# Optimization experiments

Measured on AMD Instinct MI355X. Metric: run time of the kernel, lower is better.

The kernel has to match this reference:

```python
import jax, jax.numpy as jnp
import numpy as np

BATCH = 4096
IN_DIM = 512
OUT_DIM = 512
GRID_SIZE = 5
K = 3


def _extended_grid():
    # Original: grid = linspace(-1, 1, grid_size+1), spacing h = 2/grid_size.
    # The de Boor-Cox recursion in the source indexes up to grid[grid_size+2k],
    # so we extend the uniform grid to the right with the same spacing.
    h = 2.0 / GRID_SIZE
    return (-1.0 + h * jnp.arange(GRID_SIZE + 2 * K + 1)).astype(jnp.float32)


def bspline_basis(x, grid, k):
    """Vectorized de Boor-Cox recursion.
    x: [..., ] floats; returns basis [..., grid_size + k].
    Identical math to the recursive b_spline_basis in the source, but computed
    bottom-up over all knot intervals at once (no redundant recomputation).
    """
    xe = x[..., None]  # [..., 1]
    # degree-0: indicator of half-open knot intervals, [..., n_knots-1]
    B = ((grid[:-1] <= xe) & (xe < grid[1:])).astype(x.dtype)
    for d in range(1, k + 1):
        n = grid.shape[0] - d - 1
        gi, gid = grid[:n], grid[d:d + n]          # grid[i], grid[i+d]
        gi1, gid1 = grid[1:n + 1], grid[d + 1:d + n + 1]  # grid[i+1], grid[i+d+1]
        # uniform grid -> denominators are d*h, never zero
        B = (xe - gi) / (gid - gi) * B[..., :n] + (gid1 - xe) / (gid1 - gi1) * B[..., 1:n + 1]
    return B  # [..., grid_size + k]


def setup_inputs() -> dict:
    key = jax.random.key(0)
    k1, k2 = jax.random.split(key)
    x = jax.random.uniform(k1, (BATCH, IN_DIM), jnp.float32) * 2.0 - 1.0  # in [-1, 1)
    spline_coeff = jax.random.normal(k2, (IN_DIM, OUT_DIM, GRID_SIZE + K), jnp.float32)
    spline_scaling = jnp.ones((IN_DIM, OUT_DIM), jnp.float32)
    return {"x": x, "spline_coeff": spline_coeff, "spline_scaling": spline_scaling}


def reference(x, spline_coeff, spline_scaling):
    grid = _extended_grid()
    basis = bspline_basis(x, grid, K)  # [B, in_dim, grid_size+k]
    # out[b, j] = sum_i scaling[i,j] * sum_g basis[b,i,g] * coeff[i,j,g]
    return jnp.einsum('big,ijg,ij->bj', basis, spline_coeff, spline_scaling)
```

## Files before the change

### kernel.cpp

```cpp
#include <hip/hip_runtime.h>
#include <hip/hip_bf16.h>
#include <stdint.h>


#define BATCH   4096
#define IN_DIM  512
#define OUT_DIM 512
#define KDIM    (IN_DIM * 8)
#define SPLITK  4
#define KSPAN   (KDIM / SPLITK)
#define NKS     (KSPAN / 64)

typedef short short8 __attribute__((ext_vector_type(8)));
typedef float f32x4  __attribute__((ext_vector_type(4)));

#define WAIT_VM8 0xF78
#define WAIT_VM0 0xF70

__device__ __forceinline__ unsigned short f2bf(float f) {
  union { float f; unsigned int u; } v; v.f = f;
  unsigned int r = v.u + 0x7FFFu + ((v.u >> 16) & 1u);
  return (unsigned short)(r >> 16);
}

__device__ __forceinline__ void bspline_win(float xv, float* w, int* mm) {
  float t = (xv + 1.0f) * 2.5f;
  int m = (int)t;
  m = m < 0 ? 0 : (m > 4 ? 4 : m);
  float u  = t - (float)m;
  float u2 = u * u, u3 = u2 * u, om = 1.0f - u;
  w[0] = om * om * om * (1.0f / 6.0f);
  w[1] = (3.0f * u3 - 6.0f * u2 + 4.0f) * (1.0f / 6.0f);
  w[2] = (-3.0f * u3 + 3.0f * u2 + 3.0f * u + 1.0f) * (1.0f / 6.0f);
  w[3] = u3 * (1.0f / 6.0f);
  *mm = m;
}

__device__ __forceinline__ short8 basis_pack8(float xv) {
  float w[4]; int m;
  bspline_win(xv, w, &m);
  short8 h = {};
#pragma unroll
  for (int g = 0; g < 8; ++g) {
    int d = g - m + 3;
    float v = (d == 0) ? w[0] : (d == 1) ? w[1] : (d == 2) ? w[2] : (d == 3) ? w[3] : 0.0f;
    h[g] = (short)f2bf(v);
  }
  return h;
}

__device__ __forceinline__ void async_load16(const void* g, void* l) {
  __builtin_amdgcn_global_load_lds(
      (__attribute__((address_space(1))) void*)(uintptr_t)g,
      (__attribute__((address_space(3))) void*)(unsigned int)(uintptr_t)l,
      16, 0, 0);
}

__global__ void kan_prep(const float* __restrict__ x,
                         const float* __restrict__ coeff,
                         const float* __restrict__ scaling,
                         unsigned short* __restrict__ Ag,
                         unsigned short* __restrict__ Wt) {
  const int b = blockIdx.x;
  if (b < (BATCH * IN_DIM) / 256) {
    int idx = b * 256 + threadIdx.x;
    short8 h = basis_pack8(x[idx]);
    *reinterpret_cast<short8*>(Ag + (size_t)idx * 8) = h;
  } else {
    int idx = (b - (BATCH * IN_DIM) / 256) * 256 + threadIdx.x;
    int i = idx >> 9, j = idx & 511;
    float s = scaling[idx];
    const float4* cp = reinterpret_cast<const float4*>(coeff) + (size_t)idx * 2;
    float4 c0 = cp[0], c1 = cp[1];
    short8 h;
    h[0] = (short)f2bf(c0.x * s); h[1] = (short)f2bf(c0.y * s);
    h[2] = (short)f2bf(c0.z * s); h[3] = (short)f2bf(c0.w * s);
    h[4] = (short)f2bf(c1.x * s); h[5] = (short)f2bf(c1.y * s);
    h[6] = (short)f2bf(c1.z * s); h[7] = (short)f2bf(c1.w * s);
    *reinterpret_cast<short8*>(Wt + (size_t)j * KDIM + i * 8) = h;
  }
}

__global__ __launch_bounds__(256, 2)
void kan_gemm_s(const unsigned short* __restrict__ Ag,
                const unsigned short* __restrict__ Wt,
                float* __restrict__ Pt) {
  __shared__ unsigned short As[2][128 * 64];
  __shared__ unsigned short Bs[2][128 * 64];

  const int tid  = threadIdx.x;
  const int lane = tid & 63;
  const int wid  = tid >> 6;
  const int wm = wid >> 1, wn = wid & 1;
  const int ln = lane & 15, quad = lane >> 4;

  const int b    = blockIdx.x;
  const int ks   = b & 3;
  const int mt   = (b >> 2) & 31;
  const int nt   = b >> 7;
  const int row0 = mt * 128;
  const int col0 = nt * 128;
  const int k0   = ks * KSPAN;

  f32x4 acc[4][4] = {};

  const int lr = lane >> 3;
  const int cg = (lane & 7) ^ lr;

  const unsigned short* aRow = Ag + (size_t)(row0 + wid * 32 + lr) * KDIM + k0 + cg * 8;
  const unsigned short* bRow = Wt + (size_t)(col0 + wid * 32 + lr) * KDIM + k0 + cg * 8;

  auto issue = [&](int kt, int st) {
    const int kk0 = kt * 64;
#pragma unroll
    for (int t = 0; t < 4; ++t) {
      const int rbase = wid * 32 + t * 8;
      async_load16(aRow + (size_t)t * 8 * KDIM + kk0, &As[st][rbase * 64]);
      async_load16(bRow + (size_t)t * 8 * KDIM + kk0, &Bs[st][rbase * 64]);
    }
  };

  auto compute = [&](int st) {
#pragma unroll
    for (int kk = 0; kk < 2; ++kk) {
      short8 af[4], bfr[4];
#pragma unroll
      for (int m = 0; m < 4; ++m) {
        const int r    = wm * 64 + m * 16 + ln;
        const int slot = (kk * 4 + quad) ^ (r & 7);
        af[m] = *reinterpret_cast<const short8*>(&As[st][r * 64 + slot * 8]);
      }
#pragma unroll
      for (int n = 0; n < 4; ++n) {
        const int c    = wn * 64 + n * 16 + ln;
        const int slot = (kk * 4 + quad) ^ (c & 7);
        bfr[n] = *reinterpret_cast<const short8*>(&Bs[st][c * 64 + slot * 8]);
      }
#pragma unroll
      for (int m = 0; m < 4; ++m)
#pragma unroll
        for (int n = 0; n < 4; ++n)
          acc[m][n] = __builtin_amdgcn_mfma_f32_16x16x32_bf16(af[m], bfr[n], acc[m][n], 0, 0, 0);
    }
  };

  issue(0, 0); issue(1, 1);

  for (int kt = 0; kt < NKS - 1; ++kt) {
    __builtin_amdgcn_s_waitcnt(WAIT_VM8);
    __builtin_amdgcn_s_barrier();
    compute(kt & 1);
    __builtin_amdgcn_s_barrier();
    if (kt + 2 < NKS) issue(kt + 2, kt & 1);
  }
  __builtin_amdgcn_s_waitcnt(WAIT_VM0);
  __builtin_amdgcn_s_barrier();
  compute((NKS - 1) & 1);

  float* P = Pt + (size_t)ks * BATCH * OUT_DIM;
#pragma unroll
  for (int m = 0; m < 4; ++m)
#pragma unroll
    for (int n = 0; n < 4; ++n) {
      const int col = col0 + wn * 64 + n * 16 + ln;
#pragma unroll
      for (int r = 0; r < 4; ++r) {
        const int row = row0 + wm * 64 + m * 16 + quad * 4 + r;
        P[(size_t)row * OUT_DIM + col] = acc[m][n][r];
      }
    }
}

__global__ __launch_bounds__(256)
void kan_reduce(const float* __restrict__ Pt, float* __restrict__ out) {
  const size_t Q = (size_t)BATCH * OUT_DIM / 4;
  const size_t t = (size_t)blockIdx.x * 256 + threadIdx.x;
  const float4* p = reinterpret_cast<const float4*>(Pt);
  float4 a = p[t], b = p[t + Q], c = p[t + 2 * Q], d = p[t + 3 * Q];
  float4 s;
  s.x = (a.x + b.x) + (c.x + d.x);
  s.y = (a.y + b.y) + (c.y + d.y);
  s.z = (a.z + b.z) + (c.z + d.z);
  s.w = (a.w + b.w) + (c.w + d.w);
  reinterpret_cast<float4*>(out)[t] = s;
}

__global__ __launch_bounds__(256, 2)
void kan_gemm_fb(const float* __restrict__ x, const float* __restrict__ coeff,
                 const float* __restrict__ scaling, float* __restrict__ out) {
  __shared__ unsigned short As[64 * 64];
  __shared__ unsigned short Bs[64 * 64];

  const int tid  = threadIdx.x;
  const int lane = tid & 63;
  const int wid  = tid >> 6;
  const int wm = wid >> 1, wn = wid & 1;
  const int ln = lane & 15, quad = lane >> 4;
  const int row0 = blockIdx.y * 64;
  const int col0 = blockIdx.x * 64;

  f32x4 acc[2][2] = {};

  for (int kt = 0; kt < KDIM / 64; ++kt) {
#pragma unroll
    for (int pp = 0; pp < 2; ++pp) {
      const int p  = tid + pp * 256;
      const int rn = p & 63;
      const int il = p >> 6;
      const int sw = ((il ^ (rn & 7)) * 8);
      short8 ha = basis_pack8(x[(size_t)(row0 + rn) * IN_DIM + kt * 8 + il]);
      *reinterpret_cast<short8*>(&As[rn * 64 + sw]) = ha;
      const float* cbase = coeff + (size_t)(kt * 8 + il) * 4096 + (size_t)(col0 + rn) * 8;
      float4 c0 = reinterpret_cast<const float4*>(cbase)[0];
      float4 c1 = reinterpret_cast<const float4*>(cbase)[1];
      float s = scaling[(size_t)(kt * 8 + il) * OUT_DIM + col0 + rn];
      short8 hb;
      hb[0] = (short)f2bf(c0.x * s); hb[1] = (short)f2bf(c0.y * s);
      hb[2] = (short)f2bf(c0.z * s); hb[3] = (short)f2bf(c0.w * s);
      hb[4] = (short)f2bf(c1.x * s); hb[5] = (short)f2bf(c1.y * s);
      hb[6] = (short)f2bf(c1.z * s); hb[7] = (short)f2bf(c1.w * s);
      *reinterpret_cast<short8*>(&Bs[rn * 64 + sw]) = hb;
    }
    __syncthreads();
#pragma unroll
    for (int kk = 0; kk < 2; ++kk) {
      short8 af[2], bfr[2];
#pragma unroll
      for (int mt = 0; mt < 2; ++mt) {
        const int r  = wm * 32 + mt * 16 + ln;
        const int pc = (kk * 4 + quad) ^ (r & 7);
        af[mt] = *reinterpret_cast<const short8*>(&As[r * 64 + pc * 8]);
      }
#pragma unroll
      for (int nt = 0; nt < 2; ++nt) {
        const int c  = wn * 32 + nt * 16 + ln;
        const int pc = (kk * 4 + quad) ^ (c & 7);
        bfr[nt] = *reinterpret_cast<const short8*>(&Bs[c * 64 + pc * 8]);
      }
#pragma unroll
      for (int mt = 0; mt < 2; ++mt)
#pragma unroll
        for (int nt = 0; nt < 2; ++nt)
          acc[mt][nt] = __builtin_amdgcn_mfma_f32_16x16x32_bf16(af[mt], bfr[nt], acc[mt][nt], 0, 0, 0);
    }
    __syncthreads();
  }
#pragma unroll
  for (int mt = 0; mt < 2; ++mt)
#pragma unroll
    for (int nt = 0; nt < 2; ++nt) {
      const int col = col0 + wn * 32 + nt * 16 + ln;
#pragma unroll
      for (int r = 0; r < 4; ++r) {
        const int row = row0 + wm * 32 + mt * 16 + quad * 4 + r;
        out[(size_t)row * OUT_DIM + col] = acc[mt][nt][r];
      }
    }
}

extern "C" void kernel_launch(void* const* d_in, const int* in_sizes, int n_in,
                              void* d_out, int out_size, void* d_ws, size_t ws_size,
                              hipStream_t stream) {
  const float* x       = (const float*)d_in[0];
  const float* coeff   = (const float*)d_in[1];
  const float* scaling = (const float*)d_in[2];
  float* out = (float*)d_out;

  const size_t offW = (size_t)BATCH * KDIM * 2;
  const size_t offP = offW + (size_t)OUT_DIM * KDIM * 2;
  const size_t need = offP + (size_t)SPLITK * BATCH * OUT_DIM * 4;

  if (ws_size >= need) {
    unsigned short* Ag = (unsigned short*)d_ws;
    unsigned short* Wt = (unsigned short*)((char*)d_ws + offW);
    float*          Pt = (float*)((char*)d_ws + offP);
    kan_prep<<<(BATCH * IN_DIM) / 256 + (IN_DIM * OUT_DIM) / 256, 256, 0, stream>>>(
        x, coeff, scaling, Ag, Wt);
    kan_gemm_s<<<(BATCH / 128) * (OUT_DIM / 128) * SPLITK, 256, 0, stream>>>(Ag, Wt, Pt);
    kan_reduce<<<(BATCH * OUT_DIM / 4) / 256, 256, 0, stream>>>(Pt, out);
  } else {
    kan_gemm_fb<<<dim3(OUT_DIM / 64, BATCH / 64), 256, 0, stream>>>(x, coeff, scaling, out);
  }
}
```

Baseline: 100.4 us.

## Replace split-K partial buffer and reduce kernel with atomic accumulation; restructure LDS fragment pipeline

The output is now zeroed inside the prep kernel, and each split-K GEMM block atomically adds its tile into the output. This removes the partial-sum workspace and the separate reduce kernel, saving a launch and about 32 MB of traffic. The main loop now loads all LDS fragments into registers, waits on LGKM, then issues the next async global loads before running the MFMAs, so loads overlap with math. The cost is float atomics, whose summation order is nondeterministic, and more register pressure from holding both k-halves of the fragments.

```diff
diff --git a/kernel.cpp b/kernel.cpp
--- a/kernel.cpp
+++ b/kernel.cpp
@@ -14,8 +14,9 @@
 typedef short short8 __attribute__((ext_vector_type(8)));
 typedef float f32x4  __attribute__((ext_vector_type(4)));
 
-#define WAIT_VM8 0xF78
-#define WAIT_VM0 0xF70
+#define WAIT_VM8   0xF78
+#define WAIT_VM0   0xF70
+#define WAIT_LGKM0 0xC07F
 
 __device__ __forceinline__ unsigned short f2bf(float f) {
   union { float f; unsigned int u; } v; v.f = f;
@@ -60,14 +61,17 @@
                          const float* __restrict__ coeff,
                          const float* __restrict__ scaling,
                          unsigned short* __restrict__ Ag,
-                         unsigned short* __restrict__ Wt) {
+                         unsigned short* __restrict__ Wt,
+                         float* __restrict__ out) {
   const int b = blockIdx.x;
-  if (b < (BATCH * IN_DIM) / 256) {
+  const int NB_A = (BATCH * IN_DIM) / 256;
+  const int NB_W = (IN_DIM * OUT_DIM) / 256;
+  if (b < NB_A) {
     int idx = b * 256 + threadIdx.x;
     short8 h = basis_pack8(x[idx]);
     *reinterpret_cast<short8*>(Ag + (size_t)idx * 8) = h;
-  } else {
-    int idx = (b - (BATCH * IN_DIM) / 256) * 256 + threadIdx.x;
+  } else if (b < NB_A + NB_W) {
+    int idx = (b - NB_A) * 256 + threadIdx.x;
     int i = idx >> 9, j = idx & 511;
     float s = scaling[idx];
     const float4* cp = reinterpret_cast<const float4*>(coeff) + (size_t)idx * 2;
@@ -78,13 +82,16 @@
     h[4] = (short)f2bf(c1.x * s); h[5] = (short)f2bf(c1.y * s);
     h[6] = (short)f2bf(c1.z * s); h[7] = (short)f2bf(c1.w * s);
     *reinterpret_cast<short8*>(Wt + (size_t)j * KDIM + i * 8) = h;
+  } else {
+    size_t t = (size_t)(b - NB_A - NB_W) * 256 + threadIdx.x;
+    reinterpret_cast<float4*>(out)[t] = make_float4(0.f, 0.f, 0.f, 0.f);
   }
 }
 
 __global__ __launch_bounds__(256, 2)
 void kan_gemm_s(const unsigned short* __restrict__ Ag,
                 const unsigned short* __restrict__ Wt,
-                float* __restrict__ Pt) {
+                float* __restrict__ out) {
   __shared__ unsigned short As[2][128 * 64];
   __shared__ unsigned short Bs[2][128 * 64];
 
@@ -103,6 +110,7 @@
   const int k0   = ks * KSPAN;
 
   f32x4 acc[4][4] = {};
+  short8 af[2][4], bfr[2][4];
 
   const int lr = lane >> 3;
   const int cg = (lane & 7) ^ lr;
@@ -120,28 +128,32 @@
     }
   };
 
-  auto compute = [&](int st) {
+  auto loadFrags = [&](int st) {
 #pragma unroll
     for (int kk = 0; kk < 2; ++kk) {
-      short8 af[4], bfr[4];
 #pragma unroll
       for (int m = 0; m < 4; ++m) {
         const int r    = wm * 64 + m * 16 + ln;
         const int slot = (kk * 4 + quad) ^ (r & 7);
-        af[m] = *reinterpret_cast<const short8*>(&As[st][r * 64 + slot * 8]);
+        af[kk][m] = *reinterpret_cast<const short8*>(&As[st][r * 64 + slot * 8]);
       }
 #pragma unroll
       for (int n = 0; n < 4; ++n) {
         const int c    = wn * 64 + n * 16 + ln;
         const int slot = (kk * 4 + quad) ^ (c & 7);
-        bfr[n] = *reinterpret_cast<const short8*>(&Bs[st][c * 64 + slot * 8]);
-      }
+        bfr[kk][n] = *reinterpret_cast<const short8*>(&Bs[st][c * 64 + slot * 8]);
+      }
+    }
+  };
+
+  auto mfmaAll = [&]() {
+#pragma unroll
+    for (int kk = 0; kk < 2; ++kk)
 #pragma unroll
       for (int m = 0; m < 4; ++m)
 #pragma unroll
         for (int n = 0; n < 4; ++n)
-          acc[m][n] = __builtin_amdgcn_mfma_f32_16x16x32_bf16(af[m], bfr[n], acc[m][n], 0, 0, 0);
-    }
+          acc[m][n] = __builtin_amdgcn_mfma_f32_16x16x32_bf16(af[kk][m], bfr[kk][n], acc[m][n], 0, 0, 0);
   };
 
   issue(0, 0); issue(1, 1);
@@ -149,15 +161,18 @@
   for (int kt = 0; kt < NKS - 1; ++kt) {
     __builtin_amdgcn_s_waitcnt(WAIT_VM8);
     __builtin_amdgcn_s_barrier();
-    compute(kt & 1);
+    loadFrags(kt & 1);
+    __builtin_amdgcn_s_waitcnt(WAIT_LGKM0);
+    __builtin_amdgcn_sched_barrier(0);
     __builtin_amdgcn_s_barrier();
     if (kt + 2 < NKS) issue(kt + 2, kt & 1);
+    mfmaAll();
   }
   __builtin_amdgcn_s_waitcnt(WAIT_VM0);
   __builtin_amdgcn_s_barrier();
-  compute((NKS - 1) & 1);
-
-  float* P = Pt + (size_t)ks * BATCH * OUT_DIM;
+  loadFrags((NKS - 1) & 1);
+  mfmaAll();
+
 #pragma unroll
   for (int m = 0; m < 4; ++m)
 #pragma unroll
@@ -166,23 +181,9 @@
 #pragma unroll
       for (int r = 0; r < 4; ++r) {
         const int row = row0 + wm * 64 + m * 16 + quad * 4 + r;
-        P[(size_t)row * OUT_DIM + col] = acc[m][n][r];
-      }
-    }
-}
-
-__global__ __launch_bounds__(256)
-void kan_reduce(const float* __restrict__ Pt, float* __restrict__ out) {
-  const size_t Q = (size_t)BATCH * OUT_DIM / 4;
-  const size_t t = (size_t)blockIdx.x * 256 + threadIdx.x;
-  const float4* p = reinterpret_cast<const float4*>(Pt);
-  float4 a = p[t], b = p[t + Q], c = p[t + 2 * Q], d = p[t + 3 * Q];
-  float4 s;
-  s.x = (a.x + b.x) + (c.x + d.x);
-  s.y = (a.y + b.y) + (c.y + d.y);
-  s.z = (a.z + b.z) + (c.z + d.z);
-  s.w = (a.w + b.w) + (c.w + d.w);
-  reinterpret_cast<float4*>(out)[t] = s;
+        atomicAdd(&out[(size_t)row * OUT_DIM + col], acc[m][n][r]);
+      }
+    }
 }
 
 __global__ __launch_bounds__(256, 2)
@@ -224,24 +225,24 @@
     __syncthreads();
 #pragma unroll
     for (int kk = 0; kk < 2; ++kk) {
-      short8 af[2], bfr[2];
+      short8 a2[2], b2[2];
 #pragma unroll
       for (int mt = 0; mt < 2; ++mt) {
         const int r  = wm * 32 + mt * 16 + ln;
         const int pc = (kk * 4 + quad) ^ (r & 7);
-        af[mt] = *reinterpret_cast<const short8*>(&As[r * 64 + pc * 8]);
+        a2[mt] = *reinterpret_cast<const short8*>(&As[r * 64 + pc * 8]);
       }
 #pragma unroll
       for (int nt = 0; nt < 2; ++nt) {
         const int c  = wn * 32 + nt * 16 + ln;
         const int pc = (kk * 4 + quad) ^ (c & 7);
-        bfr[nt] = *reinterpret_cast<const short8*>(&Bs[c * 64 + pc * 8]);
+        b2[nt] = *reinterpret_cast<const short8*>(&Bs[c * 64 + pc * 8]);
       }
 #pragma unroll
       for (int mt = 0; mt < 2; ++mt)
 #pragma unroll
         for (int nt = 0; nt < 2; ++nt)
-          acc[mt][nt] = __builtin_amdgcn_mfma_f32_16x16x32_bf16(af[mt], bfr[nt], acc[mt][nt], 0, 0, 0);
+          acc[mt][nt] = __builtin_amdgcn_mfma_f32_16x16x32_bf16(a2[mt], b2[nt], acc[mt][nt], 0, 0, 0);
     }
     __syncthreads();
   }
@@ -267,17 +268,15 @@
   float* out = (float*)d_out;
 
   const size_t offW = (size_t)BATCH * KDIM * 2;
-  const size_t offP = offW + (size_t)OUT_DIM * KDIM * 2;
-  const size_t need = offP + (size_t)SPLITK * BATCH * OUT_DIM * 4;
+  const size_t need = offW + (size_t)OUT_DIM * KDIM * 2;
 
   if (ws_size >= need) {
     unsigned short* Ag = (unsigned short*)d_ws;
     unsigned short* Wt = (unsigned short*)((char*)d_ws + offW);
-    float*          Pt = (float*)((char*)d_ws + offP);
-    kan_prep<<<(BATCH * IN_DIM) / 256 + (IN_DIM * OUT_DIM) / 256, 256, 0, stream>>>(
-        x, coeff, scaling, Ag, Wt);
-    kan_gemm_s<<<(BATCH / 128) * (OUT_DIM / 128) * SPLITK, 256, 0, stream>>>(Ag, Wt, Pt);
-    kan_reduce<<<(BATCH * OUT_DIM / 4) / 256, 256, 0, stream>>>(Pt, out);
+    const int NB = (BATCH * IN_DIM) / 256 + (IN_DIM * OUT_DIM) / 256
+                 + (BATCH * OUT_DIM / 4) / 256;
+    kan_prep<<<NB, 256, 0, stream>>>(x, coeff, scaling, Ag, Wt, out);
+    kan_gemm_s<<<(BATCH / 128) * (OUT_DIM / 128) * SPLITK, 256, 0, stream>>>(Ag, Wt, out);
   } else {
     kan_gemm_fb<<<dim3(OUT_DIM / 64, BATCH / 64), 256, 0, stream>>>(x, coeff, scaling, out);
   }
```

New measurement: 114.2 us. 13.7% more time.
